# Performance work log

Hardware: AMD Instinct MI355X
Metric: run time of the kernel (lower is better)

The kernel has to match this reference:

```python
import jax, jax.numpy as jnp
import numpy as np

B, S, D = 4, 4096, 256


def _complex_linear(x_r, x_i, w_r, w_i):
    # torch nn.Linear: y = x @ W.T ; complex mult: (Wr + i Wi)(xr + i xi)
    real = x_r @ w_r.T - x_i @ w_i.T
    imag = x_i @ w_r.T + x_r @ w_i.T
    return real, imag


def setup_inputs() -> dict:
    key = jax.random.key(0)
    ks = jax.random.split(key, 8)
    std = 1.0 / np.sqrt(D)  # ~ nn.Linear default init scale
    return {
        "query_real": jax.random.normal(ks[0], (B, S, D), jnp.float32),
        "query_imag": jax.random.normal(ks[1], (B, S, D), jnp.float32),
        "wq_real": jax.random.normal(ks[2], (D, D), jnp.float32) * std,
        "wq_imag": jax.random.normal(ks[3], (D, D), jnp.float32) * std,
        "wk_real": jax.random.normal(ks[4], (D, D), jnp.float32) * std,
        "wk_imag": jax.random.normal(ks[5], (D, D), jnp.float32) * std,
        "wv_real": jax.random.normal(ks[6], (D, D), jnp.float32) * std,
        "wv_imag": jax.random.normal(ks[7], (D, D), jnp.float32) * std,
    }


def reference(query_real, query_imag, wq_real, wq_imag, wk_real, wk_imag, wv_real, wv_imag):
    dim = query_real.shape[-1]
    scale = dim ** (-0.5)  # faithful: uses dim, not 2*dim

    q_r, q_i = _complex_linear(query_real, query_imag, wq_real, wq_imag)
    k_r, k_i = _complex_linear(query_real, query_imag, wk_real, wk_imag)
    v_r, v_i = _complex_linear(query_real, query_imag, wv_real, wv_imag)

    q_flat = jnp.concatenate([q_r, q_i], axis=-1)  # [B,S,2D]
    k_flat = jnp.concatenate([k_r, k_i], axis=-1)  # [B,S,2D]

    scores = jnp.einsum('bqd,bkd->bqk', q_flat, k_flat) * scale  # [B,S,S]
    attn = jax.nn.softmax(scores, axis=-1)

    out_r = jnp.einsum('bqk,bkd->bqd', attn, v_r)
    out_i = jnp.einsum('bqk,bkd->bqd', attn, v_i)
    return out_r, out_i, attn
```

## Files before the change

kernel.cpp:

```cpp
#include <hip/hip_runtime.h>
#include <hip/hip_fp16.h>

typedef _Float16 f16;
typedef _Float16 f16x8 __attribute__((ext_vector_type(8)));
typedef _Float16 f16x4 __attribute__((ext_vector_type(4)));
typedef float f32x4 __attribute__((ext_vector_type(4)));

#define AS1 __attribute__((address_space(1)))
#define AS3 __attribute__((address_space(3)))

__device__ __forceinline__ void g2l16(const void* g, void* l) {
  __builtin_amdgcn_global_load_lds((const AS1 void*)g, (AS3 void*)l, 16, 0, 0);
}

__device__ __forceinline__ void xcd_swz(int& bx, int& by, int& bz) {
  int gx = gridDim.x, gy = gridDim.y;
  int nwg = gx * gy * gridDim.z;
  int lin = (blockIdx.z * gy + blockIdx.y) * gx + blockIdx.x;
  int swz = (lin & 7) * (nwg >> 3) + (lin >> 3);
  bx = swz % gx;
  int t = swz / gx;
  by = t % gy;
  bz = t / gy;
}

__global__ __launch_bounds__(256) void build_xw(const float* __restrict__ qr,
                                                const float* __restrict__ qi,
                                                const float* __restrict__ wqr,
                                                const float* __restrict__ wqi,
                                                const float* __restrict__ wkr,
                                                const float* __restrict__ wki,
                                                const float* __restrict__ wvr,
                                                const float* __restrict__ wvi,
                                                f16* __restrict__ X,
                                                f16* __restrict__ W) {
  if (blockIdx.x < 8192) {
    long i = (long)blockIdx.x * 256 + threadIdx.x;
    long e = i * 4;
    int m = (int)(e >> 9);
    int k = (int)(e & 511);
    const float* src = (k < 256) ? (qr + (long)m * 256 + k)
                                 : (qi + (long)m * 256 + (k - 256));
    float4 v = *(const float4*)src;
    f16x4 h = {(f16)v.x, (f16)v.y, (f16)v.z, (f16)v.w};
    *(f16x4*)(X + e) = h;
  } else {
    long i = (long)(blockIdx.x - 8192) * 256 + threadIdx.x;
    long e = i * 4;
    int n = (int)(e >> 9);
    int k = (int)(e & 511);
    int sel = n >> 8;
    int row = n & 255;
    int k2 = k & 255;
    bool hi = (k >= 256);
    const float *Wr, *Wi;
    if ((sel >> 1) == 0)      { Wr = wqr; Wi = wqi; }
    else if ((sel >> 1) == 1) { Wr = wkr; Wi = wki; }
    else                      { Wr = wvr; Wi = wvi; }
    const float* src;
    float sgn = 1.0f;
    if ((sel & 1) == 0) {
      if (!hi) src = Wr + (long)row * 256 + k2;
      else   { src = Wi + (long)row * 256 + k2; sgn = -1.0f; }
    } else {
      if (!hi) src = Wi + (long)row * 256 + k2;
      else     src = Wr + (long)row * 256 + k2;
    }
    float4 v = *(const float4*)src;
    f16x4 h = {(f16)(sgn * v.x), (f16)(sgn * v.y), (f16)(sgn * v.z), (f16)(sgn * v.w)};
    *(f16x4*)(W + e) = h;
  }
}

template <int MODE>
__global__ __launch_bounds__(512, 4) void gemm_nt(const f16* __restrict__ A, int lda, long astr,
                                                  const f16* __restrict__ B, int ldb, long bstr,
                                                  int K, float scale,
                                                  void* __restrict__ C0, long cstr,
                                                  float2* __restrict__ stats,
                                                  f16* __restrict__ VT) {
  __shared__ __align__(16) f16 As[256 * 64];
  __shared__ __align__(16) f16 Bs[128 * 64];
  int bx, by, bz;
  xcd_swz(bx, by, bz);
  const f16* Ab = A + (long)bz * astr;
  const f16* Bb = B + (long)bz * bstr;
  const int tid = threadIdx.x;
  const int wave = tid >> 6, lane = tid & 63;
  const int bm = by * 256, bn = bx * 128;
  const int wm = (wave >> 1) * 64, wn = (wave & 1) * 64;
  const int lr = lane & 15, lg = lane >> 4;

  const int srow = wave * 8 + (lane >> 3);
  const int sk = ((lane & 7) ^ (lane >> 3)) * 8;

  f32x4 acc[4][4] = {};

  for (int kt = 0; kt < K; kt += 64) {
#pragma unroll
    for (int it = 0; it < 4; ++it)
      g2l16(Ab + (long)(bm + srow + it * 64) * lda + kt + sk,
            (char*)As + it * 8192 + wave * 1024);
#pragma unroll
    for (int it = 0; it < 2; ++it)
      g2l16(Bb + (long)(bn + srow + it * 64) * ldb + kt + sk,
            (char*)Bs + it * 8192 + wave * 1024);
    __syncthreads();
#pragma unroll
    for (int kk = 0; kk < 2; ++kk) {
      f16x8 af[4], bf[4];
#pragma unroll
      for (int f = 0; f < 4; ++f) {
        int sw = ((kk * 4 + lg) ^ (lr & 7)) * 8;
        af[f] = *(const f16x8*)(As + (wm + f * 16 + lr) * 64 + sw);
        bf[f] = *(const f16x8*)(Bs + (wn + f * 16 + lr) * 64 + sw);
      }
#pragma unroll
      for (int fm = 0; fm < 4; ++fm)
#pragma unroll
        for (int fn = 0; fn < 4; ++fn)
          acc[fm][fn] = __builtin_amdgcn_mfma_f32_16x16x32_f16(af[fm], bf[fn], acc[fm][fn], 0, 0, 0);
    }
    __syncthreads();
  }

  if (MODE == 0 && bn >= 1024) {
    const int b = bm >> 12;
    const int rbase = (bm & 4095) + wm;
#pragma unroll
    for (int fm = 0; fm < 4; ++fm) {
#pragma unroll
      for (int fn = 0; fn < 4; ++fn) {
        int vcol = bn - 1024 + wn + fn * 16 + lr;
        int vrow = rbase + fm * 16 + lg * 4;
        f16x4 h = {(f16)acc[fm][fn][0], (f16)acc[fm][fn][1],
                   (f16)acc[fm][fn][2], (f16)acc[fm][fn][3]};
        *(f16x4*)(VT + ((long)b * 512 + vcol) * 4096 + vrow) = h;
      }
    }
  } else {
#pragma unroll
    for (int fm = 0; fm < 4; ++fm) {
#pragma unroll
      for (int fn = 0; fn < 4; ++fn) {
#pragma unroll
        for (int r = 0; r < 4; ++r) {
          int row = bm + wm + fm * 16 + lg * 4 + r;
          int col = bn + wn + fn * 16 + lr;
          float v = acc[fm][fn][r];
          if (MODE == 0) {
            ((f16*)C0)[(long)row * 1536 + col] = (f16)v;
          } else {
            ((f16*)C0)[(long)bz * cstr + (long)row * 4096 + col] = (f16)(v * scale);
          }
        }
      }
    }
  }

  if (MODE == 1) {
    const int nt = bx * 2 + (wn >> 6);
#pragma unroll
    for (int fm = 0; fm < 4; ++fm) {
#pragma unroll
      for (int r = 0; r < 4; ++r) {
        float v0 = acc[fm][0][r] * scale, v1 = acc[fm][1][r] * scale;
        float v2 = acc[fm][2][r] * scale, v3 = acc[fm][3][r] * scale;
        float mt = fmaxf(fmaxf(v0, v1), fmaxf(v2, v3));
#pragma unroll
        for (int off = 8; off >= 1; off >>= 1) mt = fmaxf(mt, __shfl_xor(mt, off));
        float lt = __expf(v0 - mt) + __expf(v1 - mt) + __expf(v2 - mt) + __expf(v3 - mt);
#pragma unroll
        for (int off = 8; off >= 1; off >>= 1) lt += __shfl_xor(lt, off);
        if (lr == 0) {
          int row = bm + wm + fm * 16 + lg * 4 + r;
          stats[(long)nt * 16384 + (long)bz * 4096 + row] = make_float2(mt, lt);
        }
      }
    }
  }
}

__global__ __launch_bounds__(256) void merge_stats(const float2* __restrict__ stats,
                                                   float2* __restrict__ ml) {
  long row = (long)blockIdx.x * 256 + threadIdx.x;
  float m = -1e30f;
#pragma unroll 8
  for (int i = 0; i < 64; ++i) m = fmaxf(m, stats[i * 16384 + row].x);
  float l = 0.0f;
#pragma unroll 8
  for (int i = 0; i < 64; ++i) {
    float2 s = stats[i * 16384 + row];
    l += s.y * __expf(s.x - m);
  }
  ml[row] = make_float2(m, l);
}

__global__ __launch_bounds__(512, 4) void pv_fused5(const float2* __restrict__ ml,
                                                    const f16* __restrict__ S16,
                                                    const f16* __restrict__ VT,
                                                    float* __restrict__ attn,
                                                    float* __restrict__ outR,
                                                    float* __restrict__ outI) {
  __shared__ __align__(16) f16 Ps0[64 * 64];
  __shared__ __align__(16) f16 Ps1[64 * 64];
  __shared__ __align__(16) f16 Bs0[256 * 64];
  __shared__ __align__(16) f16 Bs1[256 * 64];
  int lin = blockIdx.x;
  int swz = (lin & 7) * 64 + (lin >> 3);
  int b = swz >> 7;
  int rem = swz & 127;
  int rt = rem >> 1, ch = rem & 1;
  const int bm = rt * 64;
  const int c0 = ch * 256;

  const int tid = threadIdx.x;
  const int wave = tid >> 6, lane = tid & 63;
  const int wm2 = (wave >> 2) * 32;
  const int wn2 = (wave & 3) * 64;
  const int lr = lane & 15, lg = lane >> 4;

  const int prow = tid >> 3;
  const int pc8 = tid & 7;
  const int vrow = wave * 8 + (lane >> 3);
  const int vsw = ((lane & 7) ^ ((lane >> 3) & 7)) * 8;
  float2 mlv = ml[(long)b * 4096 + bm + prow];
  const float mrow = mlv.x;
  const float invl = 1.0f / mlv.y;

  const f16* Sb = S16 + ((long)(b * 4096 + bm + prow)) * 4096 + pc8 * 8;
  float* Ab = attn + ((long)(b * 4096 + bm + prow)) * 4096 + pc8 * 8;
  const f16* Vb = VT + (long)(b * 512 + c0) * 4096;
  const int pslot = (pc8 ^ (prow & 7)) * 8;

  f32x4 acc[2][4] = {};
  f16x8 scA, scB;

#define PV_G2L(BSBUF, KT)                                                   \
  {                                                                         \
    _Pragma("unroll")                                                       \
    for (int i = 0; i < 4; ++i)                                             \
      g2l16(Vb + (long)(i * 64 + vrow) * 4096 + (KT) + vsw,                 \
            (char*)BSBUF + i * 8192 + wave * 1024);                         \
  }

#define PV_EXP(SC, PSBUF, KT, DOST)                                         \
  {                                                                         \
    float p[8];                                                             \
    _Pragma("unroll") for (int j = 0; j < 8; ++j)                           \
      p[j] = __expf((float)SC[j] - mrow) * invl;                            \
    if (DOST) {                                                             \
      float4 w0 = {p[0], p[1], p[2], p[3]};                                 \
      float4 w1 = {p[4], p[5], p[6], p[7]};                                 \
      *(float4*)(Ab + (KT)) = w0;                                           \
      *(float4*)(Ab + (KT) + 4) = w1;                                       \
    }                                                                       \
    f16x8 h = {(f16)p[0], (f16)p[1], (f16)p[2], (f16)p[3],                  \
               (f16)p[4], (f16)p[5], (f16)p[6], (f16)p[7]};                 \
    *(f16x8*)(PSBUF + prow * 64 + pslot) = h;                               \
  }

#define PV_MFMA(PSBUF, BSBUF)                                               \
  {                                                                         \
    __builtin_amdgcn_s_setprio(1);                                          \
    _Pragma("unroll")                                                       \
    for (int kk = 0; kk < 2; ++kk) {                                        \
      f16x8 af[2];                                                          \
      _Pragma("unroll")                                                     \
      for (int fm = 0; fm < 2; ++fm)                                        \
        af[fm] = *(const f16x8*)(PSBUF + (wm2 + fm * 16 + lr) * 64 +        \
                                 ((kk * 4 + lg) ^ (lr & 7)) * 8);           \
      f16x8 bf[4];                                                          \
      _Pragma("unroll")                                                     \
      for (int f = 0; f < 4; ++f)                                           \
        bf[f] = *(const f16x8*)(BSBUF + (wn2 + f * 16 + lr) * 64 +          \
                                ((kk * 4 + lg) ^ (lr & 7)) * 8);            \
      _Pragma("unroll")                                                     \
      for (int fm = 0; fm < 2; ++fm)                                        \
        _Pragma("unroll")                                                   \
        for (int f = 0; f < 4; ++f)                                         \
          acc[fm][f] = __builtin_amdgcn_mfma_f32_16x16x32_f16(              \
              af[fm], bf[f], acc[fm][f], 0, 0, 0);                          \
    }                                                                       \
    __builtin_amdgcn_s_setprio(0);                                          \
  }

#define PV_SYNC_(N)                                                         \
  asm volatile("s_waitcnt vmcnt(" #N ")" ::: "memory");                     \
  asm volatile("s_waitcnt lgkmcnt(0)" ::: "memory");                        \
  __builtin_amdgcn_s_barrier();                                             \
  __builtin_amdgcn_sched_barrier(0);
#define PV_SYNC(N) PV_SYNC_(N)

#define PV_TILE(T, BCUR, BNXT, PCUR, PNXT, SCONS, SLOAD, VMN, DOST)         \
  {                                                                         \
    PV_G2L(BNXT, ((T) + 1) * 64)                                            \
    SLOAD = *(const f16x8*)(Sb + ((T) + 2) * 64);                           \
    PV_MFMA(PCUR, BCUR)                                                     \
    PV_EXP(SCONS, PNXT, ((T) + 1) * 64, DOST)                               \
    PV_SYNC(VMN)                                                            \
  }

#define PV_RUN(VMF, VMP, VME, DOST)                                         \
  {                                                                         \
    PV_G2L(Bs0, 0)                                                          \
    scA = *(const f16x8*)(Sb + 0);                                          \
    scB = *(const f16x8*)(Sb + 64);                                         \
    PV_EXP(scA, Ps0, 0, DOST)                                               \
    PV_SYNC(VMP)                                                            \
    for (int t = 0; t < 62; t += 2) {                                       \
      PV_TILE(t, Bs0, Bs1, Ps0, Ps1, scB, scA, VMF, DOST)                   \
      PV_TILE(t + 1, Bs1, Bs0, Ps1, Ps0, scA, scB, VMF, DOST)               \
    }                                                                       \
    {                                                                       \
      PV_G2L(Bs1, 63 * 64)                                                  \
      PV_MFMA(Ps0, Bs0)                                                     \
      PV_EXP(scB, Ps1, 63 * 64, DOST)                                       \
      PV_SYNC(VME)                                                          \
    }                                                                       \
    PV_MFMA(Ps1, Bs1)                                                       \
  }

  if (ch == 0) {
    PV_RUN(3, 3, 2, 1)
  } else {
    PV_RUN(1, 1, 0, 0)
  }

#undef PV_RUN
#undef PV_TILE
#undef PV_SYNC
#undef PV_SYNC_
#undef PV_MFMA
#undef PV_EXP
#undef PV_G2L

  float* outp = ch ? outI : outR;
#pragma unroll
  for (int fm = 0; fm < 2; ++fm)
#pragma unroll
    for (int f = 0; f < 4; ++f)
#pragma unroll
      for (int r = 0; r < 4; ++r) {
        int row = bm + wm2 + fm * 16 + lg * 4 + r;
        int col = wn2 + f * 16 + lr;
        outp[((long)b * 4096 + row) * 256 + col] = acc[fm][f][r];
      }
}

extern "C" void kernel_launch(void* const* d_in, const int* in_sizes, int n_in,
                              void* d_out, int out_size, void* d_ws, size_t ws_size,
                              hipStream_t stream) {
  const float* qr  = (const float*)d_in[0];
  const float* qi  = (const float*)d_in[1];
  const float* wqr = (const float*)d_in[2];
  const float* wqi = (const float*)d_in[3];
  const float* wkr = (const float*)d_in[4];
  const float* wki = (const float*)d_in[5];
  const float* wvr = (const float*)d_in[6];
  const float* wvi = (const float*)d_in[7];

  float* outR = (float*)d_out;
  float* outI = outR + (size_t)4 * 4096 * 256;
  float* attn = outI + (size_t)4 * 4096 * 256;

  const size_t offX  = 0;
  const size_t offW  = offX + (size_t)16384 * 512 * 2;
  const size_t offP  = offW + (size_t)1536 * 512 * 2;
  const size_t offVT = offP + (size_t)16384 * 1536 * 2;
  const size_t offS  = offVT + (size_t)4 * 512 * 4096 * 2;

  char* ws = (char*)d_ws;
  f16* X   = (f16*)(ws + offX);
  f16* W   = (f16*)(ws + offW);
  f16* P   = (f16*)(ws + offP);
  f16* VT  = (f16*)(ws + offVT);
  f16* S16 = (f16*)(ws + offS);
  float2* stats = (float2*)X;
  float2* ml    = (float2*)W;

  build_xw<<<8960, 256, 0, stream>>>(qr, qi, wqr, wqi, wkr, wki, wvr, wvi, X, W);

  gemm_nt<0><<<dim3(12, 64, 1), 512, 0, stream>>>(X, 512, 0L, W, 512, 0L, 512, 1.0f,
                                                  (void*)P, 0L, nullptr, VT);

  gemm_nt<1><<<dim3(32, 16, 4), 512, 0, stream>>>(P, 1536, (long)4096 * 1536,
                                                  P + 512, 1536, (long)4096 * 1536,
                                                  512, 0.0625f,
                                                  (void*)S16, (long)4096 * 4096, stats, nullptr);

  merge_stats<<<64, 256, 0, stream>>>(stats, ml);

  pv_fused5<<<512, 512, 0, stream>>>(ml, S16, VT, attn, outR, outI);
}
```

Before: 341.2 us.

## Load V fragments directly from global into registers in PV kernel

The fused softmax-PV kernel no longer stages V tiles into double-buffered shared memory with global-to-LDS loads. Each wave now reads its B-operand fragments for the MFMAs straight from global memory into registers. This cuts LDS use per block substantially, which may allow more blocks per CU, and removes LDS traffic for V. In exchange, waves that share columns load the same V data twice, there is no prefetch ahead of the MFMAs so global latency is exposed, and the hand-tuned vmcnt wait counts were left unchanged.

```diff
diff --git a/kernel.cpp b/kernel.cpp
--- a/kernel.cpp
+++ b/kernel.cpp
@@ -196,7 +196,7 @@
   ml[row] = make_float2(m, l);
 }
 
-__global__ __launch_bounds__(512, 4) void pv_fused5(const float2* __restrict__ ml,
+__global__ __launch_bounds__(512, 4) void pv_fused8(const float2* __restrict__ ml,
                                                     const f16* __restrict__ S16,
                                                     const f16* __restrict__ VT,
                                                     float* __restrict__ attn,
@@ -204,8 +204,6 @@
                                                     float* __restrict__ outI) {
   __shared__ __align__(16) f16 Ps0[64 * 64];
   __shared__ __align__(16) f16 Ps1[64 * 64];
-  __shared__ __align__(16) f16 Bs0[256 * 64];
-  __shared__ __align__(16) f16 Bs1[256 * 64];
   int lin = blockIdx.x;
   int swz = (lin & 7) * 64 + (lin >> 3);
   int b = swz >> 7;
@@ -222,8 +220,6 @@
 
   const int prow = tid >> 3;
   const int pc8 = tid & 7;
-  const int vrow = wave * 8 + (lane >> 3);
-  const int vsw = ((lane & 7) ^ ((lane >> 3) & 7)) * 8;
   float2 mlv = ml[(long)b * 4096 + bm + prow];
   const float mrow = mlv.x;
   const float invl = 1.0f / mlv.y;
@@ -231,18 +227,14 @@
   const f16* Sb = S16 + ((long)(b * 4096 + bm + prow)) * 4096 + pc8 * 8;
   float* Ab = attn + ((long)(b * 4096 + bm + prow)) * 4096 + pc8 * 8;
   const f16* Vb = VT + (long)(b * 512 + c0) * 4096;
+  const f16* Vr0 = Vb + (long)(wn2 + 0 * 16 + lr) * 4096 + lg * 8;
+  const f16* Vr1 = Vb + (long)(wn2 + 1 * 16 + lr) * 4096 + lg * 8;
+  const f16* Vr2 = Vb + (long)(wn2 + 2 * 16 + lr) * 4096 + lg * 8;
+  const f16* Vr3 = Vb + (long)(wn2 + 3 * 16 + lr) * 4096 + lg * 8;
   const int pslot = (pc8 ^ (prow & 7)) * 8;
 
   f32x4 acc[2][4] = {};
   f16x8 scA, scB;
-
-#define PV_G2L(BSBUF, KT)                                                   \
-  {                                                                         \
-    _Pragma("unroll")                                                       \
-    for (int i = 0; i < 4; ++i)                                             \
-      g2l16(Vb + (long)(i * 64 + vrow) * 4096 + (KT) + vsw,                 \
-            (char*)BSBUF + i * 8192 + wave * 1024);                         \
-  }
 
 #define PV_EXP(SC, PSBUF, KT, DOST)                                         \
   {                                                                         \
@@ -260,8 +252,16 @@
     *(f16x8*)(PSBUF + prow * 64 + pslot) = h;                               \
   }
 
-#define PV_MFMA(PSBUF, BSBUF)                                               \
+#define PV_VMFMA(PSBUF, T)                                                  \
   {                                                                         \
+    f16x8 b00 = *(const f16x8*)(Vr0 + (T) * 64);                            \
+    f16x8 b01 = *(const f16x8*)(Vr1 + (T) * 64);                            \
+    f16x8 b02 = *(const f16x8*)(Vr2 + (T) * 64);                            \
+    f16x8 b03 = *(const f16x8*)(Vr3 + (T) * 64);                            \
+    f16x8 b10 = *(const f16x8*)(Vr0 + (T) * 64 + 32);                       \
+    f16x8 b11 = *(const f16x8*)(Vr1 + (T) * 64 + 32);                       \
+    f16x8 b12 = *(const f16x8*)(Vr2 + (T) * 64 + 32);                       \
+    f16x8 b13 = *(const f16x8*)(Vr3 + (T) * 64 + 32);                       \
     __builtin_amdgcn_s_setprio(1);                                          \
     _Pragma("unroll")                                                       \
     for (int kk = 0; kk < 2; ++kk) {                                        \
@@ -270,17 +270,17 @@
       for (int fm = 0; fm < 2; ++fm)                                        \
         af[fm] = *(const f16x8*)(PSBUF + (wm2 + fm * 16 + lr) * 64 +        \
                                  ((kk * 4 + lg) ^ (lr & 7)) * 8);           \
-      f16x8 bf[4];                                                          \
       _Pragma("unroll")                                                     \
-      for (int f = 0; f < 4; ++f)                                           \
-        bf[f] = *(const f16x8*)(BSBUF + (wn2 + f * 16 + lr) * 64 +          \
-                                ((kk * 4 + lg) ^ (lr & 7)) * 8);            \
-      _Pragma("unroll")                                                     \
-      for (int fm = 0; fm < 2; ++fm)                                        \
-        _Pragma("unroll")                                                   \
-        for (int f = 0; f < 4; ++f)                                         \
-          acc[fm][f] = __builtin_amdgcn_mfma_f32_16x16x32_f16(              \
-              af[fm], bf[f], acc[fm][f], 0, 0, 0);                          \
+      for (int fm = 0; fm < 2; ++fm) {                                      \
+        acc[fm][0] = __builtin_amdgcn_mfma_f32_16x16x32_f16(                \
+            af[fm], kk ? b10 : b00, acc[fm][0], 0, 0, 0);                   \
+        acc[fm][1] = __builtin_amdgcn_mfma_f32_16x16x32_f16(                \
+            af[fm], kk ? b11 : b01, acc[fm][1], 0, 0, 0);                   \
+        acc[fm][2] = __builtin_amdgcn_mfma_f32_16x16x32_f16(                \
+            af[fm], kk ? b12 : b02, acc[fm][2], 0, 0, 0);                   \
+        acc[fm][3] = __builtin_amdgcn_mfma_f32_16x16x32_f16(                \
+            af[fm], kk ? b13 : b03, acc[fm][3], 0, 0, 0);                   \
+      }                                                                     \
     }                                                                       \
     __builtin_amdgcn_s_setprio(0);                                          \
   }
@@ -292,33 +292,30 @@
   __builtin_amdgcn_sched_barrier(0);
 #define PV_SYNC(N) PV_SYNC_(N)
 
-#define PV_TILE(T, BCUR, BNXT, PCUR, PNXT, SCONS, SLOAD, VMN, DOST)         \
+#define PV_TILE(T, PCUR, PNXT, SCONS, SLOAD, VMN, DOST)                     \
   {                                                                         \
-    PV_G2L(BNXT, ((T) + 1) * 64)                                            \
     SLOAD = *(const f16x8*)(Sb + ((T) + 2) * 64);                           \
-    PV_MFMA(PCUR, BCUR)                                                     \
+    PV_VMFMA(PCUR, T)                                                       \
     PV_EXP(SCONS, PNXT, ((T) + 1) * 64, DOST)                               \
     PV_SYNC(VMN)                                                            \
   }
 
 #define PV_RUN(VMF, VMP, VME, DOST)                                         \
   {                                                                         \
-    PV_G2L(Bs0, 0)                                                          \
     scA = *(const f16x8*)(Sb + 0);                                          \
     scB = *(const f16x8*)(Sb + 64);                                         \
     PV_EXP(scA, Ps0, 0, DOST)                                               \
     PV_SYNC(VMP)                                                            \
     for (int t = 0; t < 62; t += 2) {                                       \
-      PV_TILE(t, Bs0, Bs1, Ps0, Ps1, scB, scA, VMF, DOST)                   \
-      PV_TILE(t + 1, Bs1, Bs0, Ps1, Ps0, scA, scB, VMF, DOST)               \
+      PV_TILE(t, Ps0, Ps1, scB, scA, VMF, DOST)                             \
+      PV_TILE(t + 1, Ps1, Ps0, scA, scB, VMF, DOST)                         \
     }                                                                       \
     {                                                                       \
-      PV_G2L(Bs1, 63 * 64)                                                  \
-      PV_MFMA(Ps0, Bs0)                                                     \
+      PV_VMFMA(Ps0, 62)                                                     \
       PV_EXP(scB, Ps1, 63 * 64, DOST)                                       \
       PV_SYNC(VME)                                                          \
     }                                                                       \
-    PV_MFMA(Ps1, Bs1)                                                       \
+    PV_VMFMA(Ps1, 63)                                                       \
   }
 
   if (ch == 0) {
@@ -331,9 +328,8 @@
 #undef PV_TILE
 #undef PV_SYNC
 #undef PV_SYNC_
-#undef PV_MFMA
+#undef PV_VMFMA
 #undef PV_EXP
-#undef PV_G2L
 
   float* outp = ch ? outI : outR;
 #pragma unroll
@@ -391,5 +387,5 @@
 
   merge_stats<<<64, 256, 0, stream>>>(stats, ml);
 
-  pv_fused5<<<512, 512, 0, stream>>>(ml, S16, VT, attn, outR, outI);
-}
+  pv_fused8<<<512, 512, 0, stream>>>(ml, S16, VT, attn, outR, outI);
+}
```

Result: slower. 477.9 us (+40.0%).

## Double PV kernel row tile to 128 rows to halve V reloads

Applied to the files above, without the earlier changes.

The fused softmax-normalize/PV kernel now handles 128 query rows per block instead of 64, so each wave computes a 64x64 output subtile with a 4x4 MFMA accumulator grid. Each thread processes 16 score elements per k-tile instead of 8, and the grid shrinks from 512 to 256 blocks. The aim is to halve redundant loads of the V tile per query row and raise MFMA work per LDS read. In exchange it uses more registers and LDS, drops the occupancy hint, and runs 256 blocks, which leaves fewer waves to hide memory latency.

```diff
diff --git a/kernel.cpp b/kernel.cpp
--- a/kernel.cpp
+++ b/kernel.cpp
@@ -196,45 +196,46 @@
   ml[row] = make_float2(m, l);
 }
 
-__global__ __launch_bounds__(512, 4) void pv_fused5(const float2* __restrict__ ml,
-                                                    const f16* __restrict__ S16,
-                                                    const f16* __restrict__ VT,
-                                                    float* __restrict__ attn,
-                                                    float* __restrict__ outR,
-                                                    float* __restrict__ outI) {
-  __shared__ __align__(16) f16 Ps0[64 * 64];
-  __shared__ __align__(16) f16 Ps1[64 * 64];
+__global__ __launch_bounds__(512) void pv_fused9(const float2* __restrict__ ml,
+                                                 const f16* __restrict__ S16,
+                                                 const f16* __restrict__ VT,
+                                                 float* __restrict__ attn,
+                                                 float* __restrict__ outR,
+                                                 float* __restrict__ outI) {
+  __shared__ __align__(16) f16 Ps0[128 * 64];
+  __shared__ __align__(16) f16 Ps1[128 * 64];
   __shared__ __align__(16) f16 Bs0[256 * 64];
   __shared__ __align__(16) f16 Bs1[256 * 64];
   int lin = blockIdx.x;
-  int swz = (lin & 7) * 64 + (lin >> 3);
-  int b = swz >> 7;
-  int rem = swz & 127;
+  int swz = (lin & 7) * 32 + (lin >> 3);
+  int b = swz >> 6;
+  int rem = swz & 63;
   int rt = rem >> 1, ch = rem & 1;
-  const int bm = rt * 64;
+  const int bm = rt * 128;
   const int c0 = ch * 256;
 
   const int tid = threadIdx.x;
   const int wave = tid >> 6, lane = tid & 63;
-  const int wm2 = (wave >> 2) * 32;
+  const int wm2 = (wave >> 2) * 64;
   const int wn2 = (wave & 3) * 64;
   const int lr = lane & 15, lg = lane >> 4;
 
-  const int prow = tid >> 3;
-  const int pc8 = tid & 7;
+  const int prow = tid >> 2;
+  const int pc = tid & 3;
   const int vrow = wave * 8 + (lane >> 3);
   const int vsw = ((lane & 7) ^ ((lane >> 3) & 7)) * 8;
   float2 mlv = ml[(long)b * 4096 + bm + prow];
   const float mrow = mlv.x;
   const float invl = 1.0f / mlv.y;
 
-  const f16* Sb = S16 + ((long)(b * 4096 + bm + prow)) * 4096 + pc8 * 8;
-  float* Ab = attn + ((long)(b * 4096 + bm + prow)) * 4096 + pc8 * 8;
+  const f16* Sb = S16 + ((long)(b * 4096 + bm + prow)) * 4096 + pc * 16;
+  float* Ab = attn + ((long)(b * 4096 + bm + prow)) * 4096 + pc * 16;
   const f16* Vb = VT + (long)(b * 512 + c0) * 4096;
-  const int pslot = (pc8 ^ (prow & 7)) * 8;
-
-  f32x4 acc[2][4] = {};
-  f16x8 scA, scB;
+  const int ps0 = ((pc * 2) ^ (prow & 7)) * 8;
+  const int ps1 = ((pc * 2 + 1) ^ (prow & 7)) * 8;
+
+  f32x4 acc[4][4] = {};
+  f16x8 sa0, sa1, sb0, sb1;
 
 #define PV_G2L(BSBUF, KT)                                                   \
   {                                                                         \
@@ -244,20 +245,25 @@
             (char*)BSBUF + i * 8192 + wave * 1024);                         \
   }
 
-#define PV_EXP(SC, PSBUF, KT, DOST)                                         \
+#define PV_EXP(SC0, SC1, PSBUF, KT, DOST)                                   \
   {                                                                         \
-    float p[8];                                                             \
-    _Pragma("unroll") for (int j = 0; j < 8; ++j)                           \
-      p[j] = __expf((float)SC[j] - mrow) * invl;                            \
+    float p[16];                                                            \
+    _Pragma("unroll") for (int j = 0; j < 8; ++j) {                         \
+      p[j] = __expf((float)SC0[j] - mrow) * invl;                           \
+      p[j + 8] = __expf((float)SC1[j] - mrow) * invl;                       \
+    }                                                                       \
     if (DOST) {                                                             \
-      float4 w0 = {p[0], p[1], p[2], p[3]};                                 \
-      float4 w1 = {p[4], p[5], p[6], p[7]};                                 \
-      *(float4*)(Ab + (KT)) = w0;                                           \
-      *(float4*)(Ab + (KT) + 4) = w1;                                       \
+      _Pragma("unroll") for (int q = 0; q < 4; ++q) {                       \
+        float4 w = {p[q * 4], p[q * 4 + 1], p[q * 4 + 2], p[q * 4 + 3]};    \
+        *(float4*)(Ab + (KT) + q * 4) = w;                                  \
+      }                                                                     \
     }                                                                       \
-    f16x8 h = {(f16)p[0], (f16)p[1], (f16)p[2], (f16)p[3],                  \
-               (f16)p[4], (f16)p[5], (f16)p[6], (f16)p[7]};                 \
-    *(f16x8*)(PSBUF + prow * 64 + pslot) = h;                               \
+    f16x8 h0 = {(f16)p[0], (f16)p[1], (f16)p[2], (f16)p[3],                 \
+                (f16)p[4], (f16)p[5], (f16)p[6], (f16)p[7]};                \
+    f16x8 h1 = {(f16)p[8], (f16)p[9], (f16)p[10], (f16)p[11],               \
+                (f16)p[12], (f16)p[13], (f16)p[14], (f16)p[15]};            \
+    *(f16x8*)(PSBUF + prow * 64 + ps0) = h0;                                \
+    *(f16x8*)(PSBUF + prow * 64 + ps1) = h1;                                \
   }
 
 #define PV_MFMA(PSBUF, BSBUF)                                               \
@@ -265,22 +271,19 @@
     __builtin_amdgcn_s_setprio(1);                                          \
     _Pragma("unroll")                                                       \
     for (int kk = 0; kk < 2; ++kk) {                                        \
-      f16x8 af[2];                                                          \
+      int sw = ((kk * 4 + lg) ^ (lr & 7)) * 8;                              \
+      f16x8 af[4], bf[4];                                                   \
       _Pragma("unroll")                                                     \
-      for (int fm = 0; fm < 2; ++fm)                                        \
-        af[fm] = *(const f16x8*)(PSBUF + (wm2 + fm * 16 + lr) * 64 +        \
-                                 ((kk * 4 + lg) ^ (lr & 7)) * 8);           \
-      f16x8 bf[4];                                                          \
+      for (int f = 0; f < 4; ++f) {                                         \
+        af[f] = *(const f16x8*)(PSBUF + (wm2 + f * 16 + lr) * 64 + sw);     \
+        bf[f] = *(const f16x8*)(BSBUF + (wn2 + f * 16 + lr) * 64 + sw);     \
+      }                                                                     \
       _Pragma("unroll")                                                     \
-      for (int f = 0; f < 4; ++f)                                           \
-        bf[f] = *(const f16x8*)(BSBUF + (wn2 + f * 16 + lr) * 64 +          \
-                                ((kk * 4 + lg) ^ (lr & 7)) * 8);            \
-      _Pragma("unroll")                                                     \
-      for (int fm = 0; fm < 2; ++fm)                                        \
+      for (int fm = 0; fm < 4; ++fm)                                        \
         _Pragma("unroll")                                                   \
-        for (int f = 0; f < 4; ++f)                                         \
-          acc[fm][f] = __builtin_amdgcn_mfma_f32_16x16x32_f16(              \
-              af[fm], bf[f], acc[fm][f], 0, 0, 0);                          \
+        for (int fn = 0; fn < 4; ++fn)                                      \
+          acc[fm][fn] = __builtin_amdgcn_mfma_f32_16x16x32_f16(             \
+              af[fm], bf[fn], acc[fm][fn], 0, 0, 0);                        \
     }                                                                       \
     __builtin_amdgcn_s_setprio(0);                                          \
   }
@@ -292,39 +295,42 @@
   __builtin_amdgcn_sched_barrier(0);
 #define PV_SYNC(N) PV_SYNC_(N)
 
-#define PV_TILE(T, BCUR, BNXT, PCUR, PNXT, SCONS, SLOAD, VMN, DOST)         \
+#define PV_TILE(T, BCUR, BNXT, PCUR, PNXT, SC0, SC1, SL0, SL1, VMN, DOST)   \
   {                                                                         \
     PV_G2L(BNXT, ((T) + 1) * 64)                                            \
-    SLOAD = *(const f16x8*)(Sb + ((T) + 2) * 64);                           \
+    SL0 = *(const f16x8*)(Sb + ((T) + 2) * 64);                             \
+    SL1 = *(const f16x8*)(Sb + ((T) + 2) * 64 + 8);                         \
     PV_MFMA(PCUR, BCUR)                                                     \
-    PV_EXP(SCONS, PNXT, ((T) + 1) * 64, DOST)                               \
+    PV_EXP(SC0, SC1, PNXT, ((T) + 1) * 64, DOST)                            \
     PV_SYNC(VMN)                                                            \
   }
 
 #define PV_RUN(VMF, VMP, VME, DOST)                                         \
   {                                                                         \
     PV_G2L(Bs0, 0)                                                          \
-    scA = *(const f16x8*)(Sb + 0);                                          \
-    scB = *(const f16x8*)(Sb + 64);                                         \
-    PV_EXP(scA, Ps0, 0, DOST)                                               \
+    sa0 = *(const f16x8*)(Sb + 0);                                          \
+    sa1 = *(const f16x8*)(Sb + 8);                                          \
+    sb0 = *(const f16x8*)(Sb + 64);                                         \
+    sb1 = *(const f16x8*)(Sb + 64 + 8);                                     \
+    PV_EXP(sa0, sa1, Ps0, 0, DOST)                                          \
     PV_SYNC(VMP)                                                            \
     for (int t = 0; t < 62; t += 2) {                                       \
-      PV_TILE(t, Bs0, Bs1, Ps0, Ps1, scB, scA, VMF, DOST)                   \
-      PV_TILE(t + 1, Bs1, Bs0, Ps1, Ps0, scA, scB, VMF, DOST)               \
+      PV_TILE(t, Bs0, Bs1, Ps0, Ps1, sb0, sb1, sa0, sa1, VMF, DOST)         \
+      PV_TILE(t + 1, Bs1, Bs0, Ps1, Ps0, sa0, sa1, sb0, sb1, VMF, DOST)     \
     }                                                                       \
     {                                                                       \
       PV_G2L(Bs1, 63 * 64)                                                  \
       PV_MFMA(Ps0, Bs0)                                                     \
-      PV_EXP(scB, Ps1, 63 * 64, DOST)                                       \
+      PV_EXP(sb0, sb1, Ps1, 63 * 64, DOST)                                  \
       PV_SYNC(VME)                                                          \
     }                                                                       \
     PV_MFMA(Ps1, Bs1)                                                       \
   }
 
   if (ch == 0) {
-    PV_RUN(3, 3, 2, 1)
+    PV_RUN(6, 6, 4, 1)
   } else {
-    PV_RUN(1, 1, 0, 0)
+    PV_RUN(2, 2, 0, 0)
   }
 
 #undef PV_RUN
@@ -337,14 +343,14 @@
 
   float* outp = ch ? outI : outR;
 #pragma unroll
-  for (int fm = 0; fm < 2; ++fm)
-#pragma unroll
-    for (int f = 0; f < 4; ++f)
+  for (int fm = 0; fm < 4; ++fm)
+#pragma unroll
+    for (int fn = 0; fn < 4; ++fn)
 #pragma unroll
       for (int r = 0; r < 4; ++r) {
         int row = bm + wm2 + fm * 16 + lg * 4 + r;
-        int col = wn2 + f * 16 + lr;
-        outp[((long)b * 4096 + row) * 256 + col] = acc[fm][f][r];
+        int col = wn2 + fn * 16 + lr;
+        outp[((long)b * 4096 + row) * 256 + col] = acc[fm][fn][r];
       }
 }
 
@@ -391,5 +397,5 @@
 
   merge_stats<<<64, 256, 0, stream>>>(stats, ml);
 
-  pv_fused5<<<512, 512, 0, stream>>>(ml, S16, VT, attn, outR, outI);
-}
+  pv_fused9<<<256, 512, 0, stream>>>(ml, S16, VT, attn, outR, outI);
+}
```

Result: slower. 371.3 us (+8.8%).
